# Kernel tuning notes

Measured on AMD Instinct MI355X. Metric: run time of the kernel, lower is better.

Reference implementation:

```python
import jax, jax.numpy as jnp
import numpy as np

B, C, S = 2, 256, 24          # batch, hidden_size (channels), cube side
N = S * S * S                 # input_size = number of tokens (13824)
NH = 4                        # num_heads
DH = C // NH                  # head dim
P = 64                        # proj_size (low-rank K/V)
G = C // 32                   # conv groups in MHCResBlock
EPS_LN = 1e-5


def _lrelu(z):
    return jnp.where(z >= 0, z, 0.01 * z)


def _inorm(z):
    # instance norm over spatial dim, per (batch, channel); z: [B,C,N]
    m = jnp.mean(z, axis=-1, keepdims=True)
    v = jnp.var(z, axis=-1, keepdims=True)
    return (z - m) * jax.lax.rsqrt(v + EPS_LN)


def _gconv(z, w, b):
    # grouped 1x1x1 conv as per-group channel matmul; z: [B,C,N], w: [G,cin_g,cout_g]
    g, cin_g, cout_g = w.shape
    zg = z.reshape(z.shape[0], g, cin_g, z.shape[-1])
    out = jnp.einsum('bgin,gio->bgon', zg, w).reshape(z.shape[0], g * cout_g, z.shape[-1])
    return out + b[None, :, None]


def _ln(z, g, b):
    m = jnp.mean(z, axis=-1, keepdims=True)
    v = jnp.var(z, axis=-1, keepdims=True)
    return (z - m) * jax.lax.rsqrt(v + EPS_LN) * g + b


def _forward(x, pos_embed, ln_g, ln_b, gamma, temperature2, w_qkv, w_e, b_e,
             w_pool, b_pool, w_fc1, w_fc2, w_out1, b_out1, w_out2, b_out2,
             w_conv1, b_conv1, w_conv2, b_conv2):
    b_, c_, h_, w_, d_ = x.shape
    n_ = h_ * w_ * d_
    xf = x.reshape(b_, c_, n_)                      # [B,C,N]

    # MHCResBlock (UnetResBlock with grouped 1x1x1 convs + instance norm + lrelu)
    hdd = _lrelu(_inorm(_gconv(xf, w_conv1, b_conv1)))
    hdd = _inorm(_gconv(hdd, w_conv2, b_conv2))
    xc = _lrelu(hdd + xf)                           # [B,C,N]

    # tokens + pos embed + shared LayerNorm
    xt = xf.transpose(0, 2, 1) + pos_embed          # [B,N,C]
    xct = xc.transpose(0, 2, 1) + pos_embed
    x_n = _ln(xt, ln_g, ln_b)
    xc_n = _ln(xct, ln_g, ln_b)

    # QKV
    qkv = (x_n @ w_qkv).reshape(b_, n_, 3, NH, DH).transpose(2, 0, 3, 1, 4)  # [3,B,h,N,d]
    q, k, v = qkv[0], qkv[1], qkv[2]                # [B,h,N,d]
    qT = q.transpose(0, 1, 3, 2)                    # [B,h,d,N]
    kT = k.transpose(0, 1, 3, 2)
    vT = v.transpose(0, 1, 3, 2)

    # shared low-rank projection E == F over token dim (pre-normalization, as in source)
    k_proj = kT @ w_e + b_e                         # [B,h,d,P]
    v_proj = vT @ w_e + b_e                         # [B,h,d,P]

    # L2-normalize q over token dim (torch F.normalize eps=1e-12)
    qn = qT / jnp.maximum(jnp.linalg.norm(qT, axis=-1, keepdims=True), 1e-12)

    # channel attention: pool over tokens -> gated MLP -> sigmoid gate
    pooled = (xc_n.transpose(0, 2, 1) @ w_pool + b_pool).transpose(0, 2, 1)  # [B,1,C]
    gate = jax.nn.sigmoid(jax.nn.relu(pooled @ w_fc1) @ w_fc2)               # [B,1,C]
    x_CA = xc_n * gate                              # [B,N,C] (dropout = identity, eval)

    # spatial attention with projected K/V and per-head temperature
    attn = jnp.einsum('bhdn,bhdp->bhnp', qn, k_proj) * temperature2          # [B,h,N,P]
    attn = jax.nn.softmax(attn, axis=-1)
    x_SA = jnp.einsum('bhnp,bhdp->bhnd', attn, v_proj)                        # [B,h,N,d]
    # faithful permute(0,3,1,2).reshape(B,N,C) scramble from the source
    x_SA = x_SA.transpose(0, 3, 1, 2).reshape(b_, n_, c_)

    x_SA = x_SA @ w_out1 + b_out1                   # [B,N,C/2]
    x_CA = x_CA @ w_out2 + b_out2                   # [B,N,C/2]
    x_att = jnp.concatenate([x_SA, x_CA], axis=-1)  # [B,N,C]
    out = x_n + gamma * x_att
    return out.reshape(b_, h_, w_, d_, c_).transpose(0, 4, 1, 2, 3)


def setup_inputs() -> dict:
    key = jax.random.key(0)
    ks = jax.random.split(key, 16)
    f = lambda k, shape, sc=0.02: jax.random.normal(k, shape, jnp.float32) * sc
    return {
        'x': jax.random.normal(ks[0], (B, C, S, S, S), jnp.float32),
        'pos_embed': f(ks[1], (1, N, C)),
        'ln_g': jnp.ones((C,), jnp.float32),
        'ln_b': jnp.zeros((C,), jnp.float32),
        'gamma': jnp.full((C,), 1e-6, jnp.float32),
        'temperature2': jnp.ones((NH, 1, 1), jnp.float32),
        'w_qkv': f(ks[2], (C, 3 * C)),
        'w_e': f(ks[3], (N, P), 0.01),
        'b_e': jnp.zeros((P,), jnp.float32),
        'w_pool': f(ks[4], (N, 1), 0.01),
        'b_pool': jnp.zeros((1,), jnp.float32),
        'w_fc1': f(ks[5], (C, DH)),
        'w_fc2': f(ks[6], (DH, C)),
        'w_out1': f(ks[7], (C, C // 2)),
        'b_out1': jnp.zeros((C // 2,), jnp.float32),
        'w_out2': f(ks[8], (C, C // 2)),
        'b_out2': jnp.zeros((C // 2,), jnp.float32),
        'w_conv1': f(ks[9], (G, 32, 32), 0.1),
        'b_conv1': jnp.zeros((C,), jnp.float32),
        'w_conv2': f(ks[10], (G, 32, 32), 0.1),
        'b_conv2': jnp.zeros((C,), jnp.float32),
    }


def reference(x, pos_embed, ln_g, ln_b, gamma, temperature2, w_qkv, w_e, b_e,
              w_pool, b_pool, w_fc1, w_fc2, w_out1, b_out1, w_out2, b_out2,
              w_conv1, b_conv1, w_conv2, b_conv2):
    return _forward(x, pos_embed, ln_g, ln_b, gamma, temperature2, w_qkv, w_e, b_e,
                    w_pool, b_pool, w_fc1, w_fc2, w_out1, b_out1, w_out2, b_out2,
                    w_conv1, b_conv1, w_conv2, b_conv2)
```

## Files before the change

kernel.cpp:

```cpp
#include <hip/hip_runtime.h>
#include <hip/hip_bf16.h>
#include <math.h>

#define Bn 2
#define Cn 256
#define Nn 13824
#define NHn 4
#define Pn 64
#define Gn 8
#define NCH 54

typedef __bf16 bf16x8 __attribute__((ext_vector_type(8)));
typedef unsigned short us8v __attribute__((ext_vector_type(8)));
typedef float f32x4 __attribute__((ext_vector_type(4)));

__device__ __forceinline__ unsigned short f2bf(float f) {
  __hip_bfloat16 h = __float2bfloat16(f);
  return __builtin_bit_cast(unsigned short, h);
}
__device__ __forceinline__ float bf2f(unsigned short u) {
  return __builtin_bit_cast(float, ((unsigned)u) << 16);
}
__device__ __forceinline__ unsigned pk2(float a, float b) {
  return (unsigned)f2bf(a) | ((unsigned)f2bf(b) << 16);
}

__global__ __launch_bounds__(256) void k_transpose_pos(const float* __restrict__ pos,
                                                       float* __restrict__ posT) {
  __shared__ float tile[64][65];
  int n0 = blockIdx.x * 64;
  int c0 = blockIdx.y * 64;
  int tc = threadIdx.x & 63;
  int tr = threadIdx.x >> 6;
  #pragma unroll
  for (int k = 0; k < 16; k++) {
    int n = tr + k * 4;
    tile[n][tc] = pos[(size_t)(n0 + n) * Cn + c0 + tc];
  }
  __syncthreads();
  #pragma unroll
  for (int k = 0; k < 16; k++) {
    int c = tr + k * 4;
    posT[(size_t)(c0 + c) * Nn + n0 + tc] = tile[tc][c];
  }
}

__global__ __launch_bounds__(256) void k_wcvt(const float* __restrict__ wqkv,
                                              const float* __restrict__ w1,
                                              unsigned short* __restrict__ wqT,
                                              unsigned short* __restrict__ w1T) {
  int j = blockIdx.x, c = threadIdx.x;
  if (j < 256) wqT[(size_t)j * 256 + c] = f2bf(wqkv[(size_t)c * 768 + j]);
  else w1T[(size_t)(j - 256) * 256 + c] = f2bf(w1[(size_t)c * 128 + (j - 256)]);
}

template <bool NORM>
__global__ __launch_bounds__(256) void k_gconv(const float* __restrict__ src,
                                               const float* __restrict__ wt,
                                               const float* __restrict__ bias,
                                               const float* __restrict__ stats,
                                               float* __restrict__ dst) {
  int chunk = blockIdx.x, g = blockIdx.y, b = blockIdx.z;
  int t = threadIdx.x;
  int n = chunk * 256 + t;
  __shared__ float ws[32][32];
  __shared__ float ms[32], rs[32], bs[32];
  #pragma unroll
  for (int i = 0; i < 4; i++) {
    int e = t + 256 * i;
    ws[e >> 5][e & 31] = wt[g * 1024 + e];
  }
  if (t < 32) {
    bs[t] = bias[g * 32 + t];
    if (NORM) {
      ms[t] = stats[(b * Cn + g * 32 + t) * 2 + 0];
      rs[t] = stats[(b * Cn + g * 32 + t) * 2 + 1];
    }
  }
  __syncthreads();
  float in[32];
  const float* sp = src + ((size_t)b * Cn + g * 32) * Nn + n;
  #pragma unroll
  for (int i = 0; i < 32; i++) {
    float v = sp[(size_t)i * Nn];
    if (NORM) {
      v = (v - ms[i]) * rs[i];
      v = v >= 0.f ? v : 0.01f * v;
    }
    in[i] = v;
  }
  float* dp = dst + ((size_t)b * Cn + g * 32) * Nn + n;
  #pragma unroll
  for (int o = 0; o < 32; o++) {
    float acc = bs[o];
    #pragma unroll
    for (int i = 0; i < 32; i++) acc = fmaf(in[i], ws[i][o], acc);
    dp[(size_t)o * Nn] = acc;
  }
}

__global__ __launch_bounds__(256) void k_rowstats(const float* __restrict__ src,
                                                  float* __restrict__ stats) {
  int row = blockIdx.x;
  const float4* p = (const float4*)(src + (size_t)row * Nn);
  float s = 0.f, s2 = 0.f;
  for (int i = threadIdx.x; i < Nn / 4; i += 256) {
    float4 v = p[i];
    s += v.x + v.y + v.z + v.w;
    s2 += v.x * v.x + v.y * v.y + v.z * v.z + v.w * v.w;
  }
  #pragma unroll
  for (int off = 32; off > 0; off >>= 1) {
    s += __shfl_down(s, off);
    s2 += __shfl_down(s2, off);
  }
  __shared__ float r1[4], r2[4];
  int w = threadIdx.x >> 6;
  if ((threadIdx.x & 63) == 0) { r1[w] = s; r2[w] = s2; }
  __syncthreads();
  if (threadIdx.x == 0) {
    s = r1[0] + r1[1] + r1[2] + r1[3];
    s2 = r2[0] + r2[1] + r2[2] + r2[3];
    float m = s * (1.f / Nn);
    float var = s2 * (1.f / Nn) - m * m;
    stats[row * 2 + 0] = m;
    stats[row * 2 + 1] = rsqrtf(var + 1e-5f);
  }
}

__global__ __launch_bounds__(256) void k_fused_ln(
    const float* __restrict__ x, const float* __restrict__ t3,
    const float* __restrict__ posT, const float* __restrict__ stats3,
    const float* __restrict__ g, const float* __restrict__ beta,
    float* __restrict__ xnf, unsigned short* __restrict__ xnbf,
    unsigned short* __restrict__ xcnbf) {
  int b = blockIdx.y, n0 = blockIdx.x * 64;
  int t = threadIdx.x, lane = t & 63, q = t >> 6;
  __shared__ float red[4][64][2];
  __shared__ unsigned short T[64][264];
  int n = n0 + lane;
  float s = 0.f, ss = 0.f;
  #pragma unroll 4
  for (int ci = 0; ci < 64; ci++) {
    int c = q * 64 + ci;
    float v = x[((size_t)b * Cn + c) * Nn + n] + posT[(size_t)c * Nn + n];
    s += v; ss += v * v;
  }
  red[q][lane][0] = s; red[q][lane][1] = ss;
  __syncthreads();
  s = red[0][lane][0] + red[1][lane][0] + red[2][lane][0] + red[3][lane][0];
  ss = red[0][lane][1] + red[1][lane][1] + red[2][lane][1] + red[3][lane][1];
  float m1 = s * (1.f / 256.f);
  float r1 = rsqrtf(ss * (1.f / 256.f) - m1 * m1 + 1e-5f);
  #pragma unroll 4
  for (int ci = 0; ci < 64; ci++) {
    int c = q * 64 + ci;
    float v = x[((size_t)b * Cn + c) * Nn + n] + posT[(size_t)c * Nn + n];
    float o = (v - m1) * r1 * g[c] + beta[c];
    xnf[((size_t)b * Cn + c) * Nn + n] = o;
    T[lane][c] = f2bf(o);
  }
  __syncthreads();
  {
    int rn = t >> 2, cs = (t & 3) * 64;
    unsigned short* dst = xnbf + ((size_t)b * Nn + n0 + rn) * 256 + cs;
    #pragma unroll
    for (int i = 0; i < 8; i++) *(us8v*)(dst + i * 8) = *(const us8v*)(&T[rn][cs + i * 8]);
  }
  __syncthreads();
  s = 0.f; ss = 0.f;
  #pragma unroll 4
  for (int ci = 0; ci < 64; ci++) {
    int c = q * 64 + ci;
    float m3 = stats3[(b * Cn + c) * 2 + 0];
    float r3 = stats3[(b * Cn + c) * 2 + 1];
    float xv = x[((size_t)b * Cn + c) * Nn + n];
    float tv = t3[((size_t)b * Cn + c) * Nn + n];
    float xc = (tv - m3) * r3 + xv;
    xc = xc >= 0.f ? xc : 0.01f * xc;
    float v = xc + posT[(size_t)c * Nn + n];
    s += v; ss += v * v;
  }
  red[q][lane][0] = s; red[q][lane][1] = ss;
  __syncthreads();
  s = red[0][lane][0] + red[1][lane][0] + red[2][lane][0] + red[3][lane][0];
  ss = red[0][lane][1] + red[1][lane][1] + red[2][lane][1] + red[3][lane][1];
  float m2 = s * (1.f / 256.f);
  float r2 = rsqrtf(ss * (1.f / 256.f) - m2 * m2 + 1e-5f);
  #pragma unroll 4
  for (int ci = 0; ci < 64; ci++) {
    int c = q * 64 + ci;
    float m3 = stats3[(b * Cn + c) * 2 + 0];
    float r3 = stats3[(b * Cn + c) * 2 + 1];
    float xv = x[((size_t)b * Cn + c) * Nn + n];
    float tv = t3[((size_t)b * Cn + c) * Nn + n];
    float xc = (tv - m3) * r3 + xv;
    xc = xc >= 0.f ? xc : 0.01f * xc;
    float v = xc + posT[(size_t)c * Nn + n];
    float o = (v - m2) * r2 * g[c] + beta[c];
    T[lane][c] = f2bf(o);
  }
  __syncthreads();
  {
    int rn = t >> 2, cs = (t & 3) * 64;
    unsigned short* dst = xcnbf + ((size_t)b * Nn + n0 + rn) * 256 + cs;
    #pragma unroll
    for (int i = 0; i < 8; i++) *(us8v*)(dst + i * 8) = *(const us8v*)(&T[rn][cs + i * 8]);
  }
}

__global__ __launch_bounds__(256) void k_gemm_q(
    const unsigned short* __restrict__ Aw,
    const unsigned short* __restrict__ Bx,
    unsigned short* __restrict__ qo,
    float* __restrict__ qsq) {
  __shared__ char lds[24576];
  int b = blockIdx.z, n0 = blockIdx.x * 128, j0 = blockIdx.y * 64;
  int t = threadIdx.x, lane = t & 63, wid = t >> 6;
  int wj = wid >> 1, wt = wid & 1;
  f32x4 acc[2][4];
  #pragma unroll
  for (int i = 0; i < 2; i++)
    #pragma unroll
    for (int j = 0; j < 4; j++) acc[i][j] = (f32x4){0.f, 0.f, 0.f, 0.f};
  for (int k0 = 0; k0 < 256; k0 += 64) {
    {
      int r = t >> 2, off = (t & 3) * 16;
      const unsigned short* ga = Aw + (size_t)(j0 + r) * 256 + k0 + off;
      #pragma unroll
      for (int i = 0; i < 2; i++)
        *(us8v*)(lds + r * 128 + ((off * 2 + 16 * i) ^ ((r & 7) << 4))) = *(const us8v*)(ga + i * 8);
      int rb = t >> 1, offb = (t & 1) * 32;
      const unsigned short* gb = Bx + ((size_t)b * Nn + n0 + rb) * 256 + k0 + offb;
      #pragma unroll
      for (int i = 0; i < 4; i++)
        *(us8v*)(lds + 8192 + rb * 128 + ((offb * 2 + 16 * i) ^ ((rb & 7) << 4))) = *(const us8v*)(gb + i * 8);
    }
    __syncthreads();
    #pragma unroll
    for (int ks = 0; ks < 2; ks++) {
      int kb = ks * 64 + (lane >> 4) * 16;
      bf16x8 af[2], bfr[4];
      #pragma unroll
      for (int mt = 0; mt < 2; mt++) {
        int row = wj * 32 + mt * 16 + (lane & 15);
        af[mt] = *(bf16x8*)(lds + row * 128 + (kb ^ ((row & 7) << 4)));
      }
      #pragma unroll
      for (int tt = 0; tt < 4; tt++) {
        int row = wt * 64 + tt * 16 + (lane & 15);
        bfr[tt] = *(bf16x8*)(lds + 8192 + row * 128 + (kb ^ ((row & 7) << 4)));
      }
      #pragma unroll
      for (int mt = 0; mt < 2; mt++)
        #pragma unroll
        for (int tt = 0; tt < 4; tt++)
          acc[mt][tt] = __builtin_amdgcn_mfma_f32_16x16x32_bf16(af[mt], bfr[tt], acc[mt][tt], 0, 0, 0);
    }
    __syncthreads();
  }
  #pragma unroll
  for (int mt = 0; mt < 2; mt++)
    #pragma unroll
    for (int r = 0; r < 4; r++) {
      float v = 0.f;
      #pragma unroll
      for (int tt = 0; tt < 4; tt++) { float e = acc[mt][tt][r]; v = fmaf(e, e, v); }
      #pragma unroll
      for (int m = 1; m < 16; m <<= 1) v += __shfl_xor(v, m);
      if ((lane & 15) == 0)
        atomicAdd(&qsq[b * Cn + j0 + wj * 32 + mt * 16 + (lane >> 4) * 4 + r], v);
    }
  unsigned short* O = (unsigned short*)lds;
  #pragma unroll
  for (int mt = 0; mt < 2; mt++)
    #pragma unroll
    for (int tt = 0; tt < 4; tt++) {
      int tok = wt * 64 + tt * 16 + (lane & 15);
      int jb = wj * 32 + mt * 16 + ((lane >> 4) << 2);
      uint2 v;
      v.x = pk2(acc[mt][tt][0], acc[mt][tt][1]);
      v.y = pk2(acc[mt][tt][2], acc[mt][tt][3]);
      *(uint2*)(O + tok * 72 + jb) = v;
    }
  __syncthreads();
  int tok = t >> 1, js = (t & 1) * 32;
  unsigned short* dst = qo + ((size_t)b * Nn + n0 + tok) * 256 + j0 + js;
  #pragma unroll
  for (int i = 0; i < 4; i++) *(us8v*)(dst + i * 8) = *(const us8v*)(O + tok * 72 + js + i * 8);
}

__global__ __launch_bounds__(256) void k_xe_partial(const float* __restrict__ A,
                                                    const float* __restrict__ We,
                                                    float* __restrict__ part) {
  int chunk = blockIdx.x, ct = blockIdx.y, b = blockIdx.z;
  int c0 = ct * 64, nb = chunk * 256;
  __shared__ float As[64][17];
  __shared__ float Ws[16][64];
  int t = threadIdx.x, tx = t & 15, ty = t >> 4;
  float acc[4][4] = {};
  const float* Ab = A + (size_t)b * Cn * Nn;
  for (int k0 = 0; k0 < 256; k0 += 16) {
    {
      int cc = t >> 2, kk0 = (t & 3) * 4;
      float4 v = *(const float4*)(Ab + (size_t)(c0 + cc) * Nn + nb + k0 + kk0);
      As[cc][kk0 + 0] = v.x; As[cc][kk0 + 1] = v.y;
      As[cc][kk0 + 2] = v.z; As[cc][kk0 + 3] = v.w;
    }
    *(float4*)(&Ws[ty][tx * 4]) = *(const float4*)(We + (size_t)(nb + k0 + ty) * Pn + tx * 4);
    __syncthreads();
    #pragma unroll
    for (int kk = 0; kk < 16; kk++) {
      float a_[4], w_[4];
      #pragma unroll
      for (int i = 0; i < 4; i++) a_[i] = As[ty * 4 + i][kk];
      float4 wv = *(const float4*)(&Ws[kk][tx * 4]);
      w_[0] = wv.x; w_[1] = wv.y; w_[2] = wv.z; w_[3] = wv.w;
      #pragma unroll
      for (int i = 0; i < 4; i++)
        #pragma unroll
        for (int j = 0; j < 4; j++) acc[i][j] = fmaf(a_[i], w_[j], acc[i][j]);
    }
    __syncthreads();
  }
  #pragma unroll
  for (int i = 0; i < 4; i++) {
    float4 v = {acc[i][0], acc[i][1], acc[i][2], acc[i][3]};
    *(float4*)(part + (((size_t)(b * NCH + chunk) * Cn + c0 + ty * 4 + i) * Pn) + tx * 4) = v;
  }
}

__global__ __launch_bounds__(256) void k_xe_reduce(const float* __restrict__ part,
                                                   float* __restrict__ xe) {
  int i = blockIdx.x * 256 + threadIdx.x;
  int b = i / (Cn * Pn);
  int cp = i % (Cn * Pn);
  float s = 0.f;
  for (int ch = 0; ch < NCH; ch++) s += part[(size_t)(b * NCH + ch) * Cn * Pn + cp];
  xe[i] = s;
}

__global__ __launch_bounds__(256) void k_kvproj(const float* __restrict__ xe,
                                                const float* __restrict__ wqkv,
                                                const float* __restrict__ be,
                                                const float* __restrict__ qsq,
                                                const float* __restrict__ temp,
                                                unsigned short* __restrict__ kvp) {
  int hd = blockIdx.x * 4 + (threadIdx.x >> 6);
  int kv = blockIdx.y, b = blockIdx.z;
  int p = threadIdx.x & 63;
  int col = (kv + 1) * Cn + hd;
  float acc = be[p];
  for (int c = 0; c < Cn; c++)
    acc = fmaf(xe[((size_t)b * Cn + c) * Pn + p], wqkv[(size_t)c * 768 + col], acc);
  int h = hd >> 6, d = hd & 63;
  if (kv == 0) {
    float sc = 1.f / fmaxf(sqrtf(qsq[b * Cn + hd]), 1e-12f);
    acc *= sc * temp[h];
    kvp[((size_t)(b * 4 + h)) * 4096 + p * 64 + d] = f2bf(acc);
  } else {
    kvp[32768 + ((size_t)(b * 4 + h)) * 4096 + d * 64 + p] = f2bf(acc);
  }
}

__global__ __launch_bounds__(256) void k_pooled_part(const unsigned short* __restrict__ xcn,
                                                     const float* __restrict__ wpool,
                                                     float* __restrict__ part) {
  int ch = blockIdx.x, b = blockIdx.y, t = threadIdx.x;
  float acc = 0.f;
  for (int i = 0; i < 64; i++) {
    int n = ch * 64 + i;
    float v = bf2f(xcn[((size_t)b * Nn + n) * 256 + t]);
    acc = fmaf(v, wpool[n], acc);
  }
  part[((size_t)ch * 2 + b) * 256 + t] = acc;
}

__global__ __launch_bounds__(256) void k_gate(const float* __restrict__ part,
                                              const float* __restrict__ bpool,
                                              const float* __restrict__ wfc1,
                                              const float* __restrict__ wfc2,
                                              float* __restrict__ gate) {
  int b = blockIdx.x, t = threadIdx.x;
  float s = bpool[0];
  for (int ch = 0; ch < 216; ch++) s += part[((size_t)ch * 2 + b) * 256 + t];
  __shared__ float pl[256], h1[64];
  pl[t] = s;
  __syncthreads();
  if (t < 64) {
    float a = 0.f;
    for (int c = 0; c < Cn; c++) a = fmaf(pl[c], wfc1[c * 64 + t], a);
    h1[t] = fmaxf(a, 0.f);
  }
  __syncthreads();
  float a = 0.f;
  for (int j = 0; j < 64; j++) a = fmaf(h1[j], wfc2[j * Cn + t], a);
  gate[b * Cn + t] = 1.f / (1.f + __expf(-a));
}

__global__ __launch_bounds__(256) void k_w2gT(const float* __restrict__ gate,
                                              const float* __restrict__ w2,
                                              unsigned short* __restrict__ w2gT) {
  int j = blockIdx.x, b = blockIdx.y, c = threadIdx.x;
  w2gT[((size_t)b * 128 + j) * 256 + c] = f2bf(gate[b * Cn + c] * w2[(size_t)c * 128 + j]);
}

__global__ __launch_bounds__(128) void k_attn(const unsigned short* __restrict__ qbf,
                                              const unsigned short* __restrict__ kvp,
                                              unsigned short* __restrict__ xsa) {
  __shared__ char lds[16384 + 2 * 9216];
  int nb = blockIdx.x, h = blockIdx.y, b = blockIdx.z;
  int t = threadIdx.x, lane = t & 63, w = t >> 6;
  char* kpT = lds;
  char* vp = lds + 8192;
  unsigned short* P = (unsigned short*)(lds + 16384 + w * 9216);
  const unsigned short* kg = kvp + ((size_t)(b * 4 + h)) * 4096;
  const unsigned short* vg = kvp + 32768 + ((size_t)(b * 4 + h)) * 4096;
  {
    int r = t >> 1, off = (t & 1) * 32;
    #pragma unroll
    for (int i = 0; i < 4; i++) {
      *(us8v*)(kpT + r * 128 + ((off * 2 + 16 * i) ^ ((r & 7) << 4))) = *(const us8v*)(kg + r * 64 + off + i * 8);
      *(us8v*)(vp + r * 128 + ((off * 2 + 16 * i) ^ ((r & 7) << 4))) = *(const us8v*)(vg + r * 64 + off + i * 8);
    }
  }
  __syncthreads();
  int n0 = nb * 128 + w * 64;
  bf16x8 qf[4][2];
  #pragma unroll
  for (int tt = 0; tt < 4; tt++)
    #pragma unroll
    for (int ks = 0; ks < 2; ks++) {
      int n = n0 + tt * 16 + (lane & 15);
      qf[tt][ks] = *(const bf16x8*)(qbf + ((size_t)b * Nn + n) * 256 + h * 64 + ks * 32 + (lane >> 4) * 8);
    }
  f32x4 s[4][4];
  #pragma unroll
  for (int i = 0; i < 4; i++)
    #pragma unroll
    for (int j = 0; j < 4; j++) s[i][j] = (f32x4){0.f, 0.f, 0.f, 0.f};
  #pragma unroll
  for (int ks = 0; ks < 2; ks++) {
    int kb = ks * 64 + (lane >> 4) * 16;
    #pragma unroll
    for (int mt = 0; mt < 4; mt++) {
      int row = mt * 16 + (lane & 15);
      bf16x8 a = *(bf16x8*)(kpT + row * 128 + (kb ^ ((row & 7) << 4)));
      #pragma unroll
      for (int tt = 0; tt < 4; tt++)
        s[mt][tt] = __builtin_amdgcn_mfma_f32_16x16x32_bf16(a, qf[tt][ks], s[mt][tt], 0, 0, 0);
    }
  }
  #pragma unroll
  for (int tt = 0; tt < 4; tt++) {
    float mx = -1e30f;
    #pragma unroll
    for (int mt = 0; mt < 4; mt++)
      #pragma unroll
      for (int r = 0; r < 4; r++) mx = fmaxf(mx, s[mt][tt][r]);
    mx = fmaxf(mx, __shfl_xor(mx, 16));
    mx = fmaxf(mx, __shfl_xor(mx, 32));
    float den = 0.f;
    #pragma unroll
    for (int mt = 0; mt < 4; mt++)
      #pragma unroll
      for (int r = 0; r < 4; r++) {
        float e = __expf(s[mt][tt][r] - mx);
        s[mt][tt][r] = e; den += e;
      }
    den += __shfl_xor(den, 16);
    den += __shfl_xor(den, 32);
    float inv = 1.f / den;
    #pragma unroll
    for (int mt = 0; mt < 4; mt++)
      #pragma unroll
      for (int r = 0; r < 4; r++) s[mt][tt][r] *= inv;
  }
  #pragma unroll
  for (int mt = 0; mt < 4; mt++)
    #pragma unroll
    for (int tt = 0; tt < 4; tt++) {
      int tok = tt * 16 + (lane & 15);
      int pb = mt * 16 + ((lane >> 4) << 2);
      uint2 v;
      v.x = pk2(s[mt][tt][0], s[mt][tt][1]);
      v.y = pk2(s[mt][tt][2], s[mt][tt][3]);
      *(uint2*)(P + tok * 72 + pb) = v;
    }
  bf16x8 pf[4][2];
  #pragma unroll
  for (int mt = 0; mt < 4; mt++)
    #pragma unroll
    for (int ks = 0; ks < 2; ks++)
      pf[mt][ks] = *(const bf16x8*)(P + (mt * 16 + (lane & 15)) * 72 + ks * 32 + (lane >> 4) * 8);
  f32x4 o[4][4];
  #pragma unroll
  for (int i = 0; i < 4; i++)
    #pragma unroll
    for (int j = 0; j < 4; j++) o[i][j] = (f32x4){0.f, 0.f, 0.f, 0.f};
  #pragma unroll
  for (int ks = 0; ks < 2; ks++) {
    int kb = ks * 64 + (lane >> 4) * 16;
    #pragma unroll
    for (int nt = 0; nt < 4; nt++) {
      int row = nt * 16 + (lane & 15);
      bf16x8 bfv = *(bf16x8*)(vp + row * 128 + (kb ^ ((row & 7) << 4)));
      #pragma unroll
      for (int mt = 0; mt < 4; mt++)
        o[mt][nt] = __builtin_amdgcn_mfma_f32_16x16x32_bf16(pf[mt][ks], bfv, o[mt][nt], 0, 0, 0);
    }
  }
  #pragma unroll
  for (int mt = 0; mt < 4; mt++)
    #pragma unroll
    for (int nt = 0; nt < 4; nt++) {
      int d = nt * 16 + (lane & 15);
      int tb = mt * 16 + ((lane >> 4) << 2);
      uint2 v;
      v.x = pk2(o[mt][nt][0], o[mt][nt][1]);
      v.y = pk2(o[mt][nt][2], o[mt][nt][3]);
      *(uint2*)(P + d * 72 + tb) = v;
    }
  size_t fb = (size_t)b * Cn * Nn + ((size_t)(lane * 4 + h)) * Nn + n0;
  #pragma unroll
  for (int k = 0; k < 8; k++)
    *(us8v*)(xsa + fb + k * 8) = *(const us8v*)(P + lane * 72 + k * 8);
}

__global__ __launch_bounds__(256) void k_gemm_out(
    const unsigned short* __restrict__ Aw, size_t a_bstride,
    const unsigned short* __restrict__ Bx,
    const float* __restrict__ bias, int cbase,
    const float* __restrict__ xnf, const float* __restrict__ gamma,
    float* __restrict__ outp) {
  __shared__ char lds[33792];
  int b = blockIdx.z, n0 = blockIdx.x * 128, j0 = blockIdx.y * 64;
  int t = threadIdx.x, lane = t & 63, wid = t >> 6;
  int wj = wid >> 1, wt = wid & 1;
  const unsigned short* Ab = Aw + a_bstride * b;
  f32x4 acc[2][4];
  #pragma unroll
  for (int i = 0; i < 2; i++)
    #pragma unroll
    for (int j = 0; j < 4; j++) acc[i][j] = (f32x4){0.f, 0.f, 0.f, 0.f};
  for (int k0 = 0; k0 < 256; k0 += 64) {
    {
      int r = t >> 2, off = (t & 3) * 16;
      const unsigned short* ga = Ab + (size_t)(j0 + r) * 256 + k0 + off;
      #pragma unroll
      for (int i = 0; i < 2; i++)
        *(us8v*)(lds + r * 128 + ((off * 2 + 16 * i) ^ ((r & 7) << 4))) = *(const us8v*)(ga + i * 8);
      int rb = t >> 1, offb = (t & 1) * 32;
      const unsigned short* gb = Bx + ((size_t)b * Nn + n0 + rb) * 256 + k0 + offb;
      #pragma unroll
      for (int i = 0; i < 4; i++)
        *(us8v*)(lds + 8192 + rb * 128 + ((offb * 2 + 16 * i) ^ ((rb & 7) << 4))) = *(const us8v*)(gb + i * 8);
    }
    __syncthreads();
    #pragma unroll
    for (int ks = 0; ks < 2; ks++) {
      int kb = ks * 64 + (lane >> 4) * 16;
      bf16x8 af[2], bfr[4];
      #pragma unroll
      for (int mt = 0; mt < 2; mt++) {
        int row = wj * 32 + mt * 16 + (lane & 15);
        af[mt] = *(bf16x8*)(lds + row * 128 + (kb ^ ((row & 7) << 4)));
      }
      #pragma unroll
      for (int tt = 0; tt < 4; tt++) {
        int row = wt * 64 + tt * 16 + (lane & 15);
        bfr[tt] = *(bf16x8*)(lds + 8192 + row * 128 + (kb ^ ((row & 7) << 4)));
      }
      #pragma unroll
      for (int mt = 0; mt < 2; mt++)
        #pragma unroll
        for (int tt = 0; tt < 4; tt++)
          acc[mt][tt] = __builtin_amdgcn_mfma_f32_16x16x32_bf16(af[mt], bfr[tt], acc[mt][tt], 0, 0, 0);
    }
    __syncthreads();
  }
  float* OT = (float*)lds;
  #pragma unroll
  for (int mt = 0; mt < 2; mt++)
    #pragma unroll
    for (int tt = 0; tt < 4; tt++)
      #pragma unroll
      for (int r = 0; r < 4; r++) {
        int j = wj * 32 + mt * 16 + (lane >> 4) * 4 + r;
        int tok = wt * 64 + tt * 16 + (lane & 15);
        OT[j * 132 + tok] = acc[mt][tt][r];
      }
  __syncthreads();
  int jj = t >> 2, ts = (t & 3) * 32;
  int c = cbase + j0 + jj;
  float gm = gamma[c], bi = bias[j0 + jj];
  const float* xn = xnf + ((size_t)b * Cn + c) * Nn + n0 + ts;
  float* op = outp + ((size_t)b * Cn + c) * Nn + n0 + ts;
  #pragma unroll
  for (int i = 0; i < 8; i++) {
    f32x4 v = *(const f32x4*)(&OT[jj * 132 + ts + i * 4]);
    f32x4 xv = *(const f32x4*)(xn + i * 4);
    f32x4 ov;
    #pragma unroll
    for (int e = 0; e < 4; e++) ov[e] = xv[e] + gm * (v[e] + bi);
    *(f32x4*)(op + i * 4) = ov;
  }
}

extern "C" void kernel_launch(void* const* d_in, const int* in_sizes, int n_in,
                              void* d_out, int out_size, void* d_ws, size_t ws_size,
                              hipStream_t stream) {
  const float* x      = (const float*)d_in[0];
  const float* pos    = (const float*)d_in[1];
  const float* ln_g   = (const float*)d_in[2];
  const float* ln_b   = (const float*)d_in[3];
  const float* gamma  = (const float*)d_in[4];
  const float* temp2  = (const float*)d_in[5];
  const float* w_qkv  = (const float*)d_in[6];
  const float* w_e    = (const float*)d_in[7];
  const float* b_e    = (const float*)d_in[8];
  const float* w_pool = (const float*)d_in[9];
  const float* b_pool = (const float*)d_in[10];
  const float* w_fc1  = (const float*)d_in[11];
  const float* w_fc2  = (const float*)d_in[12];
  const float* w_out1 = (const float*)d_in[13];
  const float* b_out1 = (const float*)d_in[14];
  const float* w_out2 = (const float*)d_in[15];
  const float* b_out2 = (const float*)d_in[16];
  const float* w_c1   = (const float*)d_in[17];
  const float* b_c1   = (const float*)d_in[18];
  const float* w_c2   = (const float*)d_in[19];
  const float* b_c2   = (const float*)d_in[20];
  (void)in_sizes; (void)n_in; (void)out_size; (void)ws_size;
  float* out = (float*)d_out;

  const size_t SZ = (size_t)Bn * Cn * Nn;
  const size_t NC = (size_t)Nn * Cn;
  const size_t XEP = (size_t)NCH * Bn * Cn * Pn;
  char* base = (char*)d_ws;
  size_t off = 0;
  auto alloc = [&](size_t bytes) { void* p = base + off; off += (bytes + 255) & ~(size_t)255; return p; };
  float* t3     = (float*)alloc(SZ * 4);
  float* xnf    = (float*)alloc(SZ * 4);
  float* posT   = (float*)alloc(NC * 4);
  float* xepart = (float*)alloc(XEP * 4);
  unsigned short* xnbf  = (unsigned short*)alloc(SZ * 2);
  unsigned short* xcnbf = (unsigned short*)alloc(SZ * 2);
  char* alias = (char*)alloc(SZ * 4);
  float* t1 = (float*)alias;
  unsigned short* qbf   = (unsigned short*)alias;
  unsigned short* xsabf = (unsigned short*)alias + SZ;
  float* stats1 = (float*)alloc(1024 * 4);
  float* stats3 = (float*)alloc(1024 * 4);
  float* xe     = (float*)alloc(32768 * 4);
  float* qsq    = (float*)alloc(512 * 4);
  float* ppart  = (float*)alloc(110592 * 4);
  float* gateb  = (float*)alloc(512 * 4);
  unsigned short* kvp  = (unsigned short*)alloc(65536 * 2);
  unsigned short* w2gt = (unsigned short*)alloc(65536 * 2);
  unsigned short* wqT  = (unsigned short*)alloc(65536 * 2);
  unsigned short* w1T  = (unsigned short*)alloc(32768 * 2);

  k_wcvt<<<dim3(384), 256, 0, stream>>>(w_qkv, w_out1, wqT, w1T);
  k_transpose_pos<<<dim3(216, 4), 256, 0, stream>>>(pos, posT);
  k_gconv<false><<<dim3(NCH, Gn, Bn), 256, 0, stream>>>(x, w_c1, b_c1, nullptr, t1);
  k_rowstats<<<dim3(Bn * Cn), 256, 0, stream>>>(t1, stats1);
  k_gconv<true><<<dim3(NCH, Gn, Bn), 256, 0, stream>>>(t1, w_c2, b_c2, stats1, t3);
  k_rowstats<<<dim3(Bn * Cn), 256, 0, stream>>>(t3, stats3);
  k_fused_ln<<<dim3(216, Bn), 256, 0, stream>>>(x, t3, posT, stats3, ln_g, ln_b, xnf, xnbf, xcnbf);
  hipMemsetAsync(qsq, 0, 512 * 4, stream);
  k_gemm_q<<<dim3(108, 4, Bn), 256, 0, stream>>>(wqT, xnbf, qbf, qsq);
  k_xe_partial<<<dim3(NCH, 4, Bn), 256, 0, stream>>>(xnf, w_e, xepart);
  k_xe_reduce<<<dim3(128), 256, 0, stream>>>(xepart, xe);
  k_kvproj<<<dim3(64, 2, Bn), 256, 0, stream>>>(xe, w_qkv, b_e, qsq, temp2, kvp);
  k_pooled_part<<<dim3(216, Bn), 256, 0, stream>>>(xcnbf, w_pool, ppart);
  k_gate<<<dim3(Bn), 256, 0, stream>>>(ppart, b_pool, w_fc1, w_fc2, gateb);
  k_w2gT<<<dim3(128, Bn), 256, 0, stream>>>(gateb, w_out2, w2gt);
  k_attn<<<dim3(108, NHn, Bn), 128, 0, stream>>>(qbf, kvp, xsabf);
  k_gemm_out<<<dim3(108, 2, Bn), 256, 0, stream>>>(w1T, 0, xsabf, b_out1, 0, xnf, gamma, out);
  k_gemm_out<<<dim3(108, 2, Bn), 256, 0, stream>>>(w2gt, (size_t)128 * 256, xcnbf, b_out2, 128, xnf, gamma, out);
}
```

Baseline: 390.7 us.

## Fuse instance-norm stats into gconv, pooling into LN, and use bf16 MFMA for xe

Instance-norm row statistics are now accumulated with atomics inside the grouped-conv kernels, which removes two full re-reads of the conv outputs. The LayerNorm kernel is restructured to read x, posT and t3 once with vector loads and buffer values in LDS. It also computes the pooled gate reduction with atomics, removing the separate pooled pass. The fp32 normalized activations are replaced by a bf16 channel-major copy that feeds a new MFMA-based xe projection (using a bf16-transposed w_e) and the residual in the output GEMM. This cuts memory traffic at the cost of reduced precision in the residual and projection, plus nondeterministic atomic summation order.

```diff
diff --git a/kernel.cpp b/kernel.cpp
--- a/kernel.cpp
+++ b/kernel.cpp
@@ -12,6 +12,7 @@
 
 typedef __bf16 bf16x8 __attribute__((ext_vector_type(8)));
 typedef unsigned short us8v __attribute__((ext_vector_type(8)));
+typedef unsigned short us4v __attribute__((ext_vector_type(4)));
 typedef float f32x4 __attribute__((ext_vector_type(4)));
 
 __device__ __forceinline__ unsigned short f2bf(float f) {
@@ -54,21 +55,42 @@
   else w1T[(size_t)(j - 256) * 256 + c] = f2bf(w1[(size_t)c * 128 + (j - 256)]);
 }
 
+__global__ __launch_bounds__(256) void k_wet(const float* __restrict__ we,
+                                             unsigned short* __restrict__ weT) {
+  __shared__ float tile[64][65];
+  int n0 = blockIdx.x * 64;
+  int tc = threadIdx.x & 63;
+  int tr = threadIdx.x >> 6;
+  #pragma unroll
+  for (int k = 0; k < 16; k++) {
+    int n = tr + k * 4;
+    tile[n][tc] = we[(size_t)(n0 + n) * Pn + tc];
+  }
+  __syncthreads();
+  #pragma unroll
+  for (int k = 0; k < 16; k++) {
+    int p = tr + k * 4;
+    weT[(size_t)p * Nn + n0 + tc] = f2bf(tile[tc][p]);
+  }
+}
+
 template <bool NORM>
 __global__ __launch_bounds__(256) void k_gconv(const float* __restrict__ src,
                                                const float* __restrict__ wt,
                                                const float* __restrict__ bias,
                                                const float* __restrict__ stats,
-                                               float* __restrict__ dst) {
+                                               float* __restrict__ dst,
+                                               float* __restrict__ statacc) {
   int chunk = blockIdx.x, g = blockIdx.y, b = blockIdx.z;
   int t = threadIdx.x;
   int n = chunk * 256 + t;
-  __shared__ float ws[32][32];
+  __shared__ float ws_[32][32];
   __shared__ float ms[32], rs[32], bs[32];
+  __shared__ float sred[4][32][2];
   #pragma unroll
   for (int i = 0; i < 4; i++) {
     int e = t + 256 * i;
-    ws[e >> 5][e & 31] = wt[g * 1024 + e];
+    ws_[e >> 5][e & 31] = wt[g * 1024 + e];
   }
   if (t < 32) {
     bs[t] = bias[g * 32 + t];
@@ -89,123 +111,162 @@
     }
     in[i] = v;
   }
+  int w = t >> 6, lane = t & 63;
   float* dp = dst + ((size_t)b * Cn + g * 32) * Nn + n;
   #pragma unroll
   for (int o = 0; o < 32; o++) {
     float acc = bs[o];
     #pragma unroll
-    for (int i = 0; i < 32; i++) acc = fmaf(in[i], ws[i][o], acc);
+    for (int i = 0; i < 32; i++) acc = fmaf(in[i], ws_[i][o], acc);
     dp[(size_t)o * Nn] = acc;
-  }
-}
-
-__global__ __launch_bounds__(256) void k_rowstats(const float* __restrict__ src,
-                                                  float* __restrict__ stats) {
-  int row = blockIdx.x;
-  const float4* p = (const float4*)(src + (size_t)row * Nn);
-  float s = 0.f, s2 = 0.f;
-  for (int i = threadIdx.x; i < Nn / 4; i += 256) {
-    float4 v = p[i];
-    s += v.x + v.y + v.z + v.w;
-    s2 += v.x * v.x + v.y * v.y + v.z * v.z + v.w * v.w;
-  }
-  #pragma unroll
-  for (int off = 32; off > 0; off >>= 1) {
-    s += __shfl_down(s, off);
-    s2 += __shfl_down(s2, off);
-  }
-  __shared__ float r1[4], r2[4];
-  int w = threadIdx.x >> 6;
-  if ((threadIdx.x & 63) == 0) { r1[w] = s; r2[w] = s2; }
-  __syncthreads();
-  if (threadIdx.x == 0) {
-    s = r1[0] + r1[1] + r1[2] + r1[3];
-    s2 = r2[0] + r2[1] + r2[2] + r2[3];
-    float m = s * (1.f / Nn);
-    float var = s2 * (1.f / Nn) - m * m;
-    stats[row * 2 + 0] = m;
-    stats[row * 2 + 1] = rsqrtf(var + 1e-5f);
-  }
+    float a = acc, a2 = acc * acc;
+    #pragma unroll
+    for (int off = 1; off < 64; off <<= 1) {
+      a += __shfl_xor(a, off);
+      a2 += __shfl_xor(a2, off);
+    }
+    if (lane == 0) { sred[w][o][0] = a; sred[w][o][1] = a2; }
+  }
+  __syncthreads();
+  if (t < 64) {
+    int o = t & 31, st = t >> 5;
+    float v = sred[0][o][st] + sred[1][o][st] + sred[2][o][st] + sred[3][o][st];
+    atomicAdd(&statacc[(b * Cn + g * 32 + o) * 2 + st], v);
+  }
+}
+
+__global__ __launch_bounds__(256) void k_statfin(const float* __restrict__ acc,
+                                                 float* __restrict__ stats) {
+  int r = blockIdx.x * 256 + threadIdx.x;
+  float s = acc[r * 2], ss = acc[r * 2 + 1];
+  float m = s * (1.f / Nn);
+  float var = ss * (1.f / Nn) - m * m;
+  stats[r * 2 + 0] = m;
+  stats[r * 2 + 1] = rsqrtf(var + 1e-5f);
 }
 
 __global__ __launch_bounds__(256) void k_fused_ln(
     const float* __restrict__ x, const float* __restrict__ t3,
     const float* __restrict__ posT, const float* __restrict__ stats3,
     const float* __restrict__ g, const float* __restrict__ beta,
-    float* __restrict__ xnf, unsigned short* __restrict__ xnbf,
-    unsigned short* __restrict__ xcnbf) {
-  int b = blockIdx.y, n0 = blockIdx.x * 64;
-  int t = threadIdx.x, lane = t & 63, q = t >> 6;
-  __shared__ float red[4][64][2];
-  __shared__ unsigned short T[64][264];
-  int n = n0 + lane;
-  float s = 0.f, ss = 0.f;
-  #pragma unroll 4
-  for (int ci = 0; ci < 64; ci++) {
-    int c = q * 64 + ci;
-    float v = x[((size_t)b * Cn + c) * Nn + n] + posT[(size_t)c * Nn + n];
-    s += v; ss += v * v;
-  }
-  red[q][lane][0] = s; red[q][lane][1] = ss;
-  __syncthreads();
-  s = red[0][lane][0] + red[1][lane][0] + red[2][lane][0] + red[3][lane][0];
-  ss = red[0][lane][1] + red[1][lane][1] + red[2][lane][1] + red[3][lane][1];
-  float m1 = s * (1.f / 256.f);
-  float r1 = rsqrtf(ss * (1.f / 256.f) - m1 * m1 + 1e-5f);
-  #pragma unroll 4
-  for (int ci = 0; ci < 64; ci++) {
-    int c = q * 64 + ci;
-    float v = x[((size_t)b * Cn + c) * Nn + n] + posT[(size_t)c * Nn + n];
-    float o = (v - m1) * r1 * g[c] + beta[c];
-    xnf[((size_t)b * Cn + c) * Nn + n] = o;
-    T[lane][c] = f2bf(o);
-  }
-  __syncthreads();
-  {
-    int rn = t >> 2, cs = (t & 3) * 64;
-    unsigned short* dst = xnbf + ((size_t)b * Nn + n0 + rn) * 256 + cs;
-    #pragma unroll
-    for (int i = 0; i < 8; i++) *(us8v*)(dst + i * 8) = *(const us8v*)(&T[rn][cs + i * 8]);
-  }
-  __syncthreads();
-  s = 0.f; ss = 0.f;
-  #pragma unroll 4
-  for (int ci = 0; ci < 64; ci++) {
-    int c = q * 64 + ci;
-    float m3 = stats3[(b * Cn + c) * 2 + 0];
-    float r3 = stats3[(b * Cn + c) * 2 + 1];
-    float xv = x[((size_t)b * Cn + c) * Nn + n];
-    float tv = t3[((size_t)b * Cn + c) * Nn + n];
-    float xc = (tv - m3) * r3 + xv;
-    xc = xc >= 0.f ? xc : 0.01f * xc;
-    float v = xc + posT[(size_t)c * Nn + n];
-    s += v; ss += v * v;
-  }
-  red[q][lane][0] = s; red[q][lane][1] = ss;
-  __syncthreads();
-  s = red[0][lane][0] + red[1][lane][0] + red[2][lane][0] + red[3][lane][0];
-  ss = red[0][lane][1] + red[1][lane][1] + red[2][lane][1] + red[3][lane][1];
-  float m2 = s * (1.f / 256.f);
-  float r2 = rsqrtf(ss * (1.f / 256.f) - m2 * m2 + 1e-5f);
-  #pragma unroll 4
-  for (int ci = 0; ci < 64; ci++) {
-    int c = q * 64 + ci;
-    float m3 = stats3[(b * Cn + c) * 2 + 0];
-    float r3 = stats3[(b * Cn + c) * 2 + 1];
-    float xv = x[((size_t)b * Cn + c) * Nn + n];
-    float tv = t3[((size_t)b * Cn + c) * Nn + n];
-    float xc = (tv - m3) * r3 + xv;
-    xc = xc >= 0.f ? xc : 0.01f * xc;
-    float v = xc + posT[(size_t)c * Nn + n];
-    float o = (v - m2) * r2 * g[c] + beta[c];
-    T[lane][c] = f2bf(o);
-  }
-  __syncthreads();
-  {
-    int rn = t >> 2, cs = (t & 3) * 64;
-    unsigned short* dst = xcnbf + ((size_t)b * Nn + n0 + rn) * 256 + cs;
-    #pragma unroll
-    for (int i = 0; i < 8; i++) *(us8v*)(dst + i * 8) = *(const us8v*)(&T[rn][cs + i * 8]);
+    const float* __restrict__ wpool,
+    unsigned short* __restrict__ xnbf, unsigned short* __restrict__ xnTbf,
+    unsigned short* __restrict__ xcnbf, float* __restrict__ pooledacc) {
+  int b = blockIdx.y, n0 = blockIdx.x * 32;
+  int t = threadIdx.x, tg = t & 7, cg = t >> 3;
+  int tok4 = tg * 4;
+  __shared__ float vbuf[32 * 256];
+  __shared__ float v2buf[32 * 256];
+  __shared__ float red[4][8][4][4];
+  __shared__ float tms[32][4];
+  __shared__ float gb[256], bb[256], s3m[256], s3r[256];
+  __shared__ float wp[32];
+  __shared__ unsigned short Tb[2][32][36];
+
+  gb[t] = g[t]; bb[t] = beta[t];
+  s3m[t] = stats3[(b * Cn + t) * 2 + 0];
+  s3r[t] = stats3[(b * Cn + t) * 2 + 1];
+  if (t < 32) wp[t] = wpool[n0 + t];
+  __syncthreads();
+
+  float s1[4] = {}, q1[4] = {}, s2[4] = {}, q2[4] = {};
+  #pragma unroll
+  for (int ci = 0; ci < 8; ci++) {
+    int c = ci * 32 + cg;
+    f32x4 xv = *(const f32x4*)(x + ((size_t)b * Cn + c) * Nn + n0 + tok4);
+    f32x4 pv = *(const f32x4*)(posT + (size_t)c * Nn + n0 + tok4);
+    f32x4 tv = *(const f32x4*)(t3 + ((size_t)b * Cn + c) * Nn + n0 + tok4);
+    float m3 = s3m[c], r3 = s3r[c];
+    #pragma unroll
+    for (int j = 0; j < 4; j++) {
+      float v = xv[j] + pv[j];
+      vbuf[(ci * 4 + j) * 256 + t] = v;
+      s1[j] += v; q1[j] += v * v;
+      float xcv = (tv[j] - m3) * r3 + xv[j];
+      xcv = xcv >= 0.f ? xcv : 0.01f * xcv;
+      float v2 = xcv + pv[j];
+      v2buf[(ci * 4 + j) * 256 + t] = v2;
+      s2[j] += v2; q2[j] += v2 * v2;
+    }
+  }
+  #pragma unroll
+  for (int j = 0; j < 4; j++) {
+    float a = s1[j], bq = q1[j], c2 = s2[j], d2 = q2[j];
+    #pragma unroll
+    for (int off = 8; off < 64; off <<= 1) {
+      a += __shfl_xor(a, off);
+      bq += __shfl_xor(bq, off);
+      c2 += __shfl_xor(c2, off);
+      d2 += __shfl_xor(d2, off);
+    }
+    if ((t & 63) < 8) {
+      int w = t >> 6, tgg = t & 7;
+      red[w][tgg][j][0] = a; red[w][tgg][j][1] = bq;
+      red[w][tgg][j][2] = c2; red[w][tgg][j][3] = d2;
+    }
+  }
+  __syncthreads();
+  if (t < 32) {
+    int tgg = t >> 2, j = t & 3;
+    float a = 0, bq = 0, c2 = 0, d2 = 0;
+    #pragma unroll
+    for (int w = 0; w < 4; w++) {
+      a += red[w][tgg][j][0]; bq += red[w][tgg][j][1];
+      c2 += red[w][tgg][j][2]; d2 += red[w][tgg][j][3];
+    }
+    float m1 = a * (1.f / 256.f);
+    float r1 = rsqrtf(bq * (1.f / 256.f) - m1 * m1 + 1e-5f);
+    float m2 = c2 * (1.f / 256.f);
+    float r2 = rsqrtf(d2 * (1.f / 256.f) - m2 * m2 + 1e-5f);
+    tms[t][0] = m1; tms[t][1] = r1; tms[t][2] = m2; tms[t][3] = r2;
+  }
+  __syncthreads();
+  float m1v[4], r1v[4], m2v[4], r2v[4];
+  #pragma unroll
+  for (int j = 0; j < 4; j++) {
+    m1v[j] = tms[tok4 + j][0]; r1v[j] = tms[tok4 + j][1];
+    m2v[j] = tms[tok4 + j][2]; r2v[j] = tms[tok4 + j][3];
+  }
+  int row = t >> 3, seg = t & 7;
+  #pragma unroll
+  for (int ci = 0; ci < 8; ci++) {
+    int c = ci * 32 + cg;
+    float gg = gb[c], bv = bb[c];
+    us4v o4;
+    #pragma unroll
+    for (int j = 0; j < 4; j++) {
+      float v = vbuf[(ci * 4 + j) * 256 + t];
+      o4[j] = f2bf((v - m1v[j]) * r1v[j] * gg + bv);
+    }
+    *(us4v*)(xnTbf + ((size_t)b * Cn + c) * Nn + n0 + tok4) = o4;
+    #pragma unroll
+    for (int j = 0; j < 4; j++) Tb[ci & 1][tok4 + j][cg] = o4[j];
+    __syncthreads();
+    *(us4v*)(xnbf + ((size_t)b * Nn + n0 + row) * Cn + ci * 32 + seg * 4) =
+        *(const us4v*)&Tb[ci & 1][row][seg * 4];
+  }
+  #pragma unroll
+  for (int ci = 0; ci < 8; ci++) {
+    int c = ci * 32 + cg;
+    float gg = gb[c], bv = bb[c];
+    us4v o4;
+    float pp = 0.f;
+    #pragma unroll
+    for (int j = 0; j < 4; j++) {
+      float v = v2buf[(ci * 4 + j) * 256 + t];
+      float o = (v - m2v[j]) * r2v[j] * gg + bv;
+      o4[j] = f2bf(o);
+      pp = fmaf(o, wp[tok4 + j], pp);
+    }
+    #pragma unroll
+    for (int j = 0; j < 4; j++) Tb[ci & 1][tok4 + j][cg] = o4[j];
+    pp += __shfl_xor(pp, 1);
+    pp += __shfl_xor(pp, 2);
+    pp += __shfl_xor(pp, 4);
+    __syncthreads();
+    *(us4v*)(xcnbf + ((size_t)b * Nn + n0 + row) * Cn + ci * 32 + seg * 4) =
+        *(const us4v*)&Tb[ci & 1][row][seg * 4];
+    if (tg == 0) atomicAdd(&pooledacc[b * Cn + c], pp);
   }
 }
 
@@ -290,44 +351,49 @@
   for (int i = 0; i < 4; i++) *(us8v*)(dst + i * 8) = *(const us8v*)(O + tok * 72 + js + i * 8);
 }
 
-__global__ __launch_bounds__(256) void k_xe_partial(const float* __restrict__ A,
-                                                    const float* __restrict__ We,
-                                                    float* __restrict__ part) {
+__global__ __launch_bounds__(256) void k_xe(const unsigned short* __restrict__ xnT,
+                                            const unsigned short* __restrict__ weT,
+                                            float* __restrict__ part) {
+  __shared__ char lds[16384];
   int chunk = blockIdx.x, ct = blockIdx.y, b = blockIdx.z;
   int c0 = ct * 64, nb = chunk * 256;
-  __shared__ float As[64][17];
-  __shared__ float Ws[16][64];
-  int t = threadIdx.x, tx = t & 15, ty = t >> 4;
-  float acc[4][4] = {};
-  const float* Ab = A + (size_t)b * Cn * Nn;
-  for (int k0 = 0; k0 < 256; k0 += 16) {
-    {
-      int cc = t >> 2, kk0 = (t & 3) * 4;
-      float4 v = *(const float4*)(Ab + (size_t)(c0 + cc) * Nn + nb + k0 + kk0);
-      As[cc][kk0 + 0] = v.x; As[cc][kk0 + 1] = v.y;
-      As[cc][kk0 + 2] = v.z; As[cc][kk0 + 3] = v.w;
-    }
-    *(float4*)(&Ws[ty][tx * 4]) = *(const float4*)(We + (size_t)(nb + k0 + ty) * Pn + tx * 4);
+  int t = threadIdx.x, lane = t & 63, wid = t >> 6;
+  f32x4 acc4[4];
+  #pragma unroll
+  for (int i = 0; i < 4; i++) acc4[i] = (f32x4){0.f, 0.f, 0.f, 0.f};
+  for (int k0 = 0; k0 < 256; k0 += 64) {
+    int r = t >> 2, off = (t & 3) * 16;
+    const unsigned short* ga = xnT + ((size_t)b * Cn + c0 + r) * Nn + nb + k0 + off;
+    const unsigned short* gb = weT + (size_t)r * Nn + nb + k0 + off;
+    #pragma unroll
+    for (int i = 0; i < 2; i++) {
+      *(us8v*)(lds + r * 128 + ((off * 2 + 16 * i) ^ ((r & 7) << 4))) = *(const us8v*)(ga + i * 8);
+      *(us8v*)(lds + 8192 + r * 128 + ((off * 2 + 16 * i) ^ ((r & 7) << 4))) = *(const us8v*)(gb + i * 8);
+    }
     __syncthreads();
     #pragma unroll
-    for (int kk = 0; kk < 16; kk++) {
-      float a_[4], w_[4];
-      #pragma unroll
-      for (int i = 0; i < 4; i++) a_[i] = As[ty * 4 + i][kk];
-      float4 wv = *(const float4*)(&Ws[kk][tx * 4]);
-      w_[0] = wv.x; w_[1] = wv.y; w_[2] = wv.z; w_[3] = wv.w;
-      #pragma unroll
-      for (int i = 0; i < 4; i++)
-        #pragma unroll
-        for (int j = 0; j < 4; j++) acc[i][j] = fmaf(a_[i], w_[j], acc[i][j]);
+    for (int ks = 0; ks < 2; ks++) {
+      int kb = ks * 64 + (lane >> 4) * 16;
+      int rowa = wid * 16 + (lane & 15);
+      bf16x8 a = *(bf16x8*)(lds + rowa * 128 + (kb ^ ((rowa & 7) << 4)));
+      #pragma unroll
+      for (int pt = 0; pt < 4; pt++) {
+        int rowb = pt * 16 + (lane & 15);
+        bf16x8 bv = *(bf16x8*)(lds + 8192 + rowb * 128 + (kb ^ ((rowb & 7) << 4)));
+        acc4[pt] = __builtin_amdgcn_mfma_f32_16x16x32_bf16(a, bv, acc4[pt], 0, 0, 0);
+      }
     }
     __syncthreads();
   }
-  #pragma unroll
-  for (int i = 0; i < 4; i++) {
-    float4 v = {acc[i][0], acc[i][1], acc[i][2], acc[i][3]};
-    *(float4*)(part + (((size_t)(b * NCH + chunk) * Cn + c0 + ty * 4 + i) * Pn) + tx * 4) = v;
-  }
+  size_t base = ((size_t)(b * NCH + chunk)) * (Cn * Pn);
+  #pragma unroll
+  for (int pt = 0; pt < 4; pt++)
+    #pragma unroll
+    for (int r = 0; r < 4; r++) {
+      int c = c0 + wid * 16 + (lane >> 4) * 4 + r;
+      int p = pt * 16 + (lane & 15);
+      part[base + (size_t)c * Pn + p] = acc4[pt][r];
+    }
 }
 
 __global__ __launch_bounds__(256) void k_xe_reduce(const float* __restrict__ part,
@@ -363,29 +429,14 @@
   }
 }
 
-__global__ __launch_bounds__(256) void k_pooled_part(const unsigned short* __restrict__ xcn,
-                                                     const float* __restrict__ wpool,
-                                                     float* __restrict__ part) {
-  int ch = blockIdx.x, b = blockIdx.y, t = threadIdx.x;
-  float acc = 0.f;
-  for (int i = 0; i < 64; i++) {
-    int n = ch * 64 + i;
-    float v = bf2f(xcn[((size_t)b * Nn + n) * 256 + t]);
-    acc = fmaf(v, wpool[n], acc);
-  }
-  part[((size_t)ch * 2 + b) * 256 + t] = acc;
-}
-
-__global__ __launch_bounds__(256) void k_gate(const float* __restrict__ part,
+__global__ __launch_bounds__(256) void k_gate(const float* __restrict__ pooledacc,
                                               const float* __restrict__ bpool,
                                               const float* __restrict__ wfc1,
                                               const float* __restrict__ wfc2,
                                               float* __restrict__ gate) {
   int b = blockIdx.x, t = threadIdx.x;
-  float s = bpool[0];
-  for (int ch = 0; ch < 216; ch++) s += part[((size_t)ch * 2 + b) * 256 + t];
   __shared__ float pl[256], h1[64];
-  pl[t] = s;
+  pl[t] = pooledacc[b * Cn + t] + bpool[0];
   __syncthreads();
   if (t < 64) {
     float a = 0.f;
@@ -531,7 +582,7 @@
     const unsigned short* __restrict__ Aw, size_t a_bstride,
     const unsigned short* __restrict__ Bx,
     const float* __restrict__ bias, int cbase,
-    const float* __restrict__ xnf, const float* __restrict__ gamma,
+    const unsigned short* __restrict__ xnT, const float* __restrict__ gamma,
     float* __restrict__ outp) {
   __shared__ char lds[33792];
   int b = blockIdx.z, n0 = blockIdx.x * 128, j0 = blockIdx.y * 64;
@@ -594,15 +645,15 @@
   int jj = t >> 2, ts = (t & 3) * 32;
   int c = cbase + j0 + jj;
   float gm = gamma[c], bi = bias[j0 + jj];
-  const float* xn = xnf + ((size_t)b * Cn + c) * Nn + n0 + ts;
+  const unsigned short* xn = xnT + ((size_t)b * Cn + c) * Nn + n0 + ts;
   float* op = outp + ((size_t)b * Cn + c) * Nn + n0 + ts;
   #pragma unroll
   for (int i = 0; i < 8; i++) {
     f32x4 v = *(const f32x4*)(&OT[jj * 132 + ts + i * 4]);
-    f32x4 xv = *(const f32x4*)(xn + i * 4);
+    us4v xv = *(const us4v*)(xn + i * 4);
     f32x4 ov;
     #pragma unroll
-    for (int e = 0; e < 4; e++) ov[e] = xv[e] + gm * (v[e] + bi);
+    for (int e = 0; e < 4; e++) ov[e] = bf2f(xv[e]) + gm * (v[e] + bi);
     *(f32x4*)(op + i * 4) = ov;
   }
 }
@@ -636,47 +687,52 @@
 
   const size_t SZ = (size_t)Bn * Cn * Nn;
   const size_t NC = (size_t)Nn * Cn;
-  const size_t XEP = (size_t)NCH * Bn * Cn * Pn;
   char* base = (char*)d_ws;
   size_t off = 0;
   auto alloc = [&](size_t bytes) { void* p = base + off; off += (bytes + 255) & ~(size_t)255; return p; };
   float* t3     = (float*)alloc(SZ * 4);
-  float* xnf    = (float*)alloc(SZ * 4);
+  char*  alias  = (char*)alloc(SZ * 4);
   float* posT   = (float*)alloc(NC * 4);
-  float* xepart = (float*)alloc(XEP * 4);
+  float* xepart = (float*)alloc((size_t)NCH * Bn * Cn * Pn * 4);
   unsigned short* xnbf  = (unsigned short*)alloc(SZ * 2);
+  unsigned short* xnTbf = (unsigned short*)alloc(SZ * 2);
   unsigned short* xcnbf = (unsigned short*)alloc(SZ * 2);
-  char* alias = (char*)alloc(SZ * 4);
-  float* t1 = (float*)alias;
-  unsigned short* qbf   = (unsigned short*)alias;
-  unsigned short* xsabf = (unsigned short*)alias + SZ;
+  unsigned short* weT   = (unsigned short*)alloc((size_t)Pn * Nn * 2);
+  float* zeros  = (float*)alloc(3072 * 4);
+  float* stats1acc = zeros;
+  float* stats3acc = zeros + 1024;
+  float* qsq       = zeros + 2048;
+  float* pooledacc = zeros + 2560;
   float* stats1 = (float*)alloc(1024 * 4);
   float* stats3 = (float*)alloc(1024 * 4);
   float* xe     = (float*)alloc(32768 * 4);
-  float* qsq    = (float*)alloc(512 * 4);
-  float* ppart  = (float*)alloc(110592 * 4);
   float* gateb  = (float*)alloc(512 * 4);
   unsigned short* kvp  = (unsigned short*)alloc(65536 * 2);
   unsigned short* w2gt = (unsigned short*)alloc(65536 * 2);
   unsigned short* wqT  = (unsigned short*)alloc(65536 * 2);
   unsigned short* w1T  = (unsigned short*)alloc(32768 * 2);
 
+  float* t1 = (float*)alias;
+  unsigned short* qbf   = (unsigned short*)alias;
+  unsigned short* xsabf = (unsigned short*)alias + SZ;
+
+  hipMemsetAsync(zeros, 0, 3072 * 4, stream);
   k_wcvt<<<dim3(384), 256, 0, stream>>>(w_qkv, w_out1, wqT, w1T);
+  k_wet<<<dim3(216), 256, 0, stream>>>(w_e, weT);
   k_transpose_pos<<<dim3(216, 4), 256, 0, stream>>>(pos, posT);
-  k_gconv<false><<<dim3(NCH, Gn, Bn), 256, 0, stream>>>(x, w_c1, b_c1, nullptr, t1);
-  k_rowstats<<<dim3(Bn * Cn), 256, 0, stream>>>(t1, stats1);
-  k_gconv<true><<<dim3(NCH, Gn, Bn), 256, 0, stream>>>(t1, w_c2, b_c2, stats1, t3);
-  k_rowstats<<<dim3(Bn * Cn), 256, 0, stream>>>(t3, stats3);
-  k_fused_ln<<<dim3(216, Bn), 256, 0, stream>>>(x, t3, posT, stats3, ln_g, ln_b, xnf, xnbf, xcnbf);
-  hipMemsetAsync(qsq, 0, 512 * 4, stream);
+  k_gconv<false><<<dim3(NCH, Gn, Bn), 256, 0, stream>>>(x, w_c1, b_c1, nullptr, t1, stats1acc);
+  k_statfin<<<dim3(2), 256, 0, stream>>>(stats1acc, stats1);
+  k_gconv<true><<<dim3(NCH, Gn, Bn), 256, 0, stream>>>(t1, w_c2, b_c2, stats1, t3, stats3acc);
+  k_statfin<<<dim3(2), 256, 0, stream>>>(stats3acc, stats3);
+  k_fused_ln<<<dim3(432, Bn), 256, 0, stream>>>(x, t3, posT, stats3, ln_g, ln_b, w_pool,
+                                                xnbf, xnTbf, xcnbf, pooledacc);
   k_gemm_q<<<dim3(108, 4, Bn), 256, 0, stream>>>(wqT, xnbf, qbf, qsq);
-  k_xe_partial<<<dim3(NCH, 4, Bn), 256, 0, stream>>>(xnf, w_e, xepart);
+  k_xe<<<dim3(NCH, 4, Bn), 256, 0, stream>>>(xnTbf, weT, xepart);
   k_xe_reduce<<<dim3(128), 256, 0, stream>>>(xepart, xe);
   k_kvproj<<<dim3(64, 2, Bn), 256, 0, stream>>>(xe, w_qkv, b_e, qsq, temp2, kvp);
-  k_pooled_part<<<dim3(216, Bn), 256, 0, stream>>>(xcnbf, w_pool, ppart);
-  k_gate<<<dim3(Bn), 256, 0, stream>>>(ppart, b_pool, w_fc1, w_fc2, gateb);
+  k_gate<<<dim3(Bn), 256, 0, stream>>>(pooledacc, b_pool, w_fc1, w_fc2, gateb);
   k_w2gT<<<dim3(128, Bn), 256, 0, stream>>>(gateb, w_out2, w2gt);
   k_attn<<<dim3(108, NHn, Bn), 128, 0, stream>>>(qbf, kvp, xsabf);
-  k_gemm_out<<<dim3(108, 2, Bn), 256, 0, stream>>>(w1T, 0, xsabf, b_out1, 0, xnf, gamma, out);
-  k_gemm_out<<<dim3(108, 2, Bn), 256, 0, stream>>>(w2gt, (size_t)128 * 256, xcnbf, b_out2, 128, xnf, gamma, out);
-}
+  k_gemm_out<<<dim3(108, 2, Bn), 256, 0, stream>>>(w1T, 0, xsabf, b_out1, 0, xnTbf, gamma, out);
+  k_gemm_out<<<dim3(108, 2, Bn), 256, 0, stream>>>(w2gt, (size_t)128 * 256, xcnbf, b_out2, 128, xnTbf, gamma, out);
+}
```

Result: slower. 406.6 us (+4.1%).
